# Optimization experiments

Measured on AMD Instinct MI355X. Metric: run time of the kernel, lower is better.

Reference implementation:

```python
import jax, jax.numpy as jnp
import numpy as np

TQ, TK, H, HEADS = 2048, 2048, 1024, 16

def setup_inputs() -> dict:
    key = jax.random.key(0)
    ks = jax.random.split(key, 11)
    s = 1.0 / np.sqrt(H).astype(np.float32)
    return {
        "Q": jax.random.normal(ks[0], (TQ, H), jnp.float32),
        "K": jax.random.normal(ks[1], (TK, H), jnp.float32),
        "V": jax.random.normal(ks[2], (TK, H), jnp.float32),
        "Wq": jax.random.normal(ks[3], (H, H), jnp.float32) * s,
        "bq": jax.random.normal(ks[4], (H,), jnp.float32) * s,
        "Wk": jax.random.normal(ks[5], (H, H), jnp.float32) * s,
        "bk": jax.random.normal(ks[6], (H,), jnp.float32) * s,
        "Wv": jax.random.normal(ks[7], (H, H), jnp.float32) * s,
        "bv": jax.random.normal(ks[8], (H,), jnp.float32) * s,
        # linear_out: nn.Linear(num_heads, 1) -> weight [num_heads], bias scalar
        "Wo": jax.random.normal(ks[9], (HEADS,), jnp.float32) / np.sqrt(HEADS).astype(np.float32),
        "bo": jax.random.normal(ks[10], (), jnp.float32) / np.sqrt(HEADS).astype(np.float32),
    }

def reference(Q, K, V, Wq, bq, Wk, bk, Wv, bv, Wo, bo):
    heads = Wo.shape[0]
    # relu(linear) projections
    Q_l = jax.nn.relu(Q @ Wq.T + bq)            # [Tq, H]
    K_l = jax.nn.relu(K @ Wk.T + bk)            # [Tk, H]
    V_l = jax.nn.relu(V @ Wv.T + bv)            # [Tk, H]
    Tq, Hd = Q_l.shape
    Tk = K_l.shape[0]
    d = Hd // heads                              # head dim
    Qh = Q_l.reshape(Tq, heads, d)               # split heads (torch split+cat over dim0)
    Kh = K_l.reshape(Tk, heads, d)
    # per-head scaled scores: [Tq, Tk, heads]
    scale = np.float32(1.0 / np.sqrt(d))
    scores = jnp.einsum('qhd,khd->qkh', Qh, Kh) * scale
    # learned linear combine over heads -> [Tq, Tk]
    logits = scores @ Wo + bo
    attn = jax.nn.softmax(logits, axis=1)        # softmax over Tk
    out = attn @ V_l                             # [Tq, H]
    return out, attn.T                           # attention.transpose(1,0) -> [Tk, Tq]
```

## Files before the change

kernel.cpp:

```cpp
#include <hip/hip_runtime.h>
#include <stdint.h>


#define TQ 2048
#define TK 2048
#define HD 1024

#define DEVI __device__ __forceinline__

typedef __attribute__((ext_vector_type(8))) short bf16x8;
typedef __attribute__((ext_vector_type(4))) float f32x4;
typedef __attribute__((ext_vector_type(4))) unsigned short u16x4;

DEVI unsigned short f2bf(float f) {
  uint32_t u = __builtin_bit_cast(uint32_t, f);
  u += 0x7FFFu + ((u >> 16) & 1u);
  return (unsigned short)(u >> 16);
}
DEVI float bf2f(unsigned short h) {
  uint32_t u = ((uint32_t)h) << 16;
  return __builtin_bit_cast(float, u);
}
DEVI void gload_lds16(const void* g, void* l) {
  __builtin_amdgcn_global_load_lds((const __attribute__((address_space(1))) void*)g,
                                   (__attribute__((address_space(3))) void*)l,
                                   16, 0, 0);
}
template<int N> DEVI void wait_vm() { asm volatile("s_waitcnt vmcnt(%0)" :: "n"(N) : "memory"); }
DEVI void wait_lgkm0() { asm volatile("s_waitcnt lgkmcnt(0)" ::: "memory"); }
#define SBAR() __builtin_amdgcn_s_barrier()

DEVI void stageT(const unsigned short* __restrict__ A, const unsigned short* __restrict__ B,
                 int lda, int ldb, int k0, unsigned short* buf, int tid) {
#pragma unroll
  for (int i = 0; i < 2; i++) {
    int c = i * 512 + tid;
    int r = c >> 3;
    int cs = (c & 7) ^ (r & 7);
    gload_lds16(A + (size_t)r * lda + k0 + cs * 8, buf + c * 8);
  }
#pragma unroll
  for (int i = 0; i < 2; i++) {
    int c = i * 512 + tid;
    int r = c >> 3;
    int cs = (c & 7) ^ (r & 7);
    gload_lds16(B + (size_t)r * ldb + k0 + cs * 8, buf + 8192 + c * 8);
  }
}

DEVI void computeT(const unsigned short* lA, const unsigned short* lB, f32x4 (*acc)[2],
                   int wr, int wc, int l15, int hi) {
#pragma unroll
  for (int kk = 0; kk < 2; kk++) {
    bf16x8 af[4], bfr[2];
#pragma unroll
    for (int f = 0; f < 4; f++) {
      int ra = wr * 64 + f * 16 + l15;
      int ca = (kk * 4 + hi) ^ (ra & 7);
      af[f] = *(const bf16x8*)(lA + ra * 64 + ca * 8);
    }
#pragma unroll
    for (int f = 0; f < 2; f++) {
      int rb = wc * 32 + f * 16 + l15;
      int cb = (kk * 4 + hi) ^ (rb & 7);
      bfr[f] = *(const bf16x8*)(lB + rb * 64 + cb * 8);
    }
#pragma unroll
    for (int fm = 0; fm < 4; fm++)
#pragma unroll
      for (int fn = 0; fn < 2; fn++)
        acc[fm][fn] = __builtin_amdgcn_mfma_f32_16x16x32_bf16(af[fm], bfr[fn], acc[fm][fn], 0, 0, 0);
  }
}

template<int NKT>
DEVI void mfma_pipeline(const unsigned short* __restrict__ A, const unsigned short* __restrict__ B,
                        int lda, int ldb, unsigned short* lds, f32x4 (*acc)[2]) {
  const int tid = threadIdx.x;
  const int lane = tid & 63, wave = tid >> 6;
  const int l15 = lane & 15, hi = lane >> 4;
  const int wr = wave >> 2, wc = wave & 3;

#pragma unroll
  for (int i = 0; i < 4; i++)
#pragma unroll
    for (int j = 0; j < 2; j++) acc[i][j] = (f32x4)(0.0f);

  stageT(A, B, lda, ldb, 0, lds, tid);
  stageT(A, B, lda, ldb, 64, lds + 16384, tid);

#pragma unroll 1
  for (int t = 0; t < NKT; ++t) {
    if (t < NKT - 1) wait_vm<4>();
    else wait_vm<0>();
    SBAR();
    unsigned short* buf = lds + (t & 1) * 16384;
    __builtin_amdgcn_s_setprio(1);
    computeT(buf, buf + 8192, acc, wr, wc, l15, hi);
    __builtin_amdgcn_s_setprio(0);
    wait_lgkm0();
    SBAR();
    if (t + 2 < NKT) stageT(A, B, lda, ldb, (t + 2) * 64, buf, tid);
  }
}

__global__ __launch_bounds__(512, 4)
void gemm_proj(const unsigned short* __restrict__ Qb, const unsigned short* __restrict__ Kb,
               const unsigned short* __restrict__ Vb,
               const unsigned short* __restrict__ Wqb, const unsigned short* __restrict__ Wkb,
               const unsigned short* __restrict__ Wvb,
               const float* __restrict__ bq, const float* __restrict__ bk,
               const float* __restrict__ bv, const float* __restrict__ Wo,
               unsigned short* __restrict__ Ql, unsigned short* __restrict__ Ks,
               unsigned short* __restrict__ VT) {
  __shared__ __align__(16) unsigned short lds[2 * 16384];
  const int bid = blockIdx.x;
  const int x = bid & 7, j = bid >> 3;
  const int bmz = x * 6 + (j >> 3);
  const int bn = j & 7;
  const int z = bmz >> 4;
  const int bm = bmz & 15;

  const unsigned short* A = (z == 0) ? Qb : (z == 1) ? Kb : Vb;
  const unsigned short* B = (z == 0) ? Wqb : (z == 1) ? Wkb : Wvb;
  const float* bias = (z == 0) ? bq : (z == 1) ? bk : bv;

  f32x4 acc[4][2];
  mfma_pipeline<16>(A + (size_t)bm * 128 * HD, B + (size_t)bn * 128 * HD, HD, HD, lds, acc);

  const int tid = threadIdx.x;
  const int lane = tid & 63, wave = tid >> 6;
  const int wr = wave >> 2, wc = wave & 3;
  const int l15 = lane & 15, hi = lane >> 4;
  const int row0 = bm * 128 + wr * 64;
  const int col0 = bn * 128 + wc * 32;

  if (z == 2) {
    unsigned short (*T)[132] = reinterpret_cast<unsigned short (*)[132]>(lds);
#pragma unroll
    for (int fm = 0; fm < 4; fm++)
#pragma unroll
      for (int fn = 0; fn < 2; fn++) {
        int cl = wc * 32 + fn * 16 + l15;
        float b = bias[bn * 128 + cl];
#pragma unroll
        for (int i = 0; i < 4; i++)
          T[cl][wr * 64 + fm * 16 + hi * 4 + i] = f2bf(fmaxf(acc[fm][fn][i] + b, 0.0f));
      }
    __syncthreads();
#pragma unroll
    for (int i = 0; i < 8; i++) {
      int h = i * 512 + tid;
      int c = h >> 5;
      int rq = h & 31;
      u16x4 v = *(const u16x4*)(&T[c][rq * 4]);
      *(u16x4*)(VT + (size_t)(bn * 128 + c) * TK + bm * 128 + rq * 4) = v;
    }
  } else {
#pragma unroll
    for (int fm = 0; fm < 4; fm++)
#pragma unroll
      for (int fn = 0; fn < 2; fn++) {
        int cg = col0 + fn * 16 + l15;
        int rg = row0 + fm * 16 + hi * 4;
        float b = bias[cg];
        if (z == 1) {
          float s = 0.125f * Wo[cg >> 6];
#pragma unroll
          for (int i = 0; i < 4; i++)
            Ks[(size_t)(rg + i) * HD + cg] = f2bf(fmaxf(acc[fm][fn][i] + b, 0.0f) * s);
        } else {
#pragma unroll
          for (int i = 0; i < 4; i++)
            Ql[(size_t)(rg + i) * HD + cg] = f2bf(fmaxf(acc[fm][fn][i] + b, 0.0f));
        }
      }
  }
}

__global__ __launch_bounds__(512, 4)
void gemm_logits(const unsigned short* __restrict__ Ql, const unsigned short* __restrict__ Ks,
                 float* __restrict__ C) {
  __shared__ __align__(16) unsigned short lds[2 * 16384];
  const int bid = blockIdx.x;
  const int x = bid & 7, j = bid >> 3;
  const int bm = (x & 3) * 4 + (j >> 3);
  const int bn = (x >> 2) * 8 + (j & 7);

  f32x4 acc[4][2];
  mfma_pipeline<16>(Ql + (size_t)bm * 128 * HD, Ks + (size_t)bn * 128 * HD, HD, HD, lds, acc);

  const int tid = threadIdx.x;
  const int lane = tid & 63, wave = tid >> 6;
  const int wr = wave >> 2, wc = wave & 3;
  const int l15 = lane & 15, hi = lane >> 4;
  const int row0 = bm * 128 + wr * 64;
  const int col0 = bn * 128 + wc * 32;
#pragma unroll
  for (int fm = 0; fm < 4; fm++)
#pragma unroll
    for (int fn = 0; fn < 2; fn++) {
      int cg = col0 + fn * 16 + l15;
      int rg = row0 + fm * 16 + hi * 4;
#pragma unroll
      for (int i = 0; i < 4; i++)
        C[(size_t)(rg + i) * TK + cg] = acc[fm][fn][i];
    }
}

__global__ __launch_bounds__(512, 4)
void pv_and_transpose(const unsigned short* __restrict__ attnb, const unsigned short* __restrict__ VT,
                      float* __restrict__ outp, float* __restrict__ attnT) {
  __shared__ __align__(16) unsigned short lds[2 * 16384];
  const int bid = blockIdx.x;
  const int tid = threadIdx.x;
  if (bid < 128) {
    const int x = bid & 7, j = bid >> 3;
    const int bm = (x & 3) * 4 + (j >> 2);
    const int bn = (x >> 2) * 4 + (j & 3);
    f32x4 acc[4][2];
    mfma_pipeline<32>(attnb + (size_t)bm * 128 * TK, VT + (size_t)bn * 128 * TK,
                      TK, TK, lds, acc);
    const int lane = tid & 63, wave = tid >> 6;
    const int wr = wave >> 2, wc = wave & 3;
    const int l15 = lane & 15, hi = lane >> 4;
    const int row0 = bm * 128 + wr * 64;
    const int col0 = bn * 128 + wc * 32;
#pragma unroll
    for (int fm = 0; fm < 4; fm++)
#pragma unroll
      for (int fn = 0; fn < 2; fn++) {
        int cg = col0 + fn * 16 + l15;
        int rg = row0 + fm * 16 + hi * 4;
#pragma unroll
        for (int i = 0; i < 4; i++)
          outp[(size_t)(rg + i) * HD + cg] = acc[fm][fn][i];
      }
  } else {
    unsigned short (*tile)[68] = reinterpret_cast<unsigned short (*)[68]>(lds);
    const int q0 = bid - 128;
    const int tr = (q0 >> 5) * 64;
    const int tc = (q0 & 31) * 64;
#pragma unroll
    for (int i = 0; i < 2; i++) {
      int q = i * 512 + tid;
      int r = q >> 4;
      int c4 = (q & 15) * 4;
      u16x4 v = *(const u16x4*)(attnb + (size_t)(tr + r) * TK + tc + c4);
      *(u16x4*)(&tile[r][c4]) = v;
    }
    __syncthreads();
#pragma unroll
    for (int i = 0; i < 2; i++) {
      int q = i * 512 + tid;
      int c = q >> 4;
      int r4 = (q & 15) * 4;
      f32x4 o;
#pragma unroll
      for (int jx = 0; jx < 4; jx++) o[jx] = bf2f(tile[r4 + jx][c]);
      *(f32x4*)(attnT + (size_t)(tc + c) * TQ + tr + r4) = o;
    }
  }
}

__global__ __launch_bounds__(256)
void softmax_k(const float* __restrict__ logits, unsigned short* __restrict__ attnb) {
  const int row = blockIdx.x;
  const int tid = threadIdx.x;
  const int lane = tid & 63;
  const int wave = tid >> 6;
  const float* lr = logits + (size_t)row * TK;

  f32x4 v0 = *(const f32x4*)(lr + tid * 8);
  f32x4 v1 = *(const f32x4*)(lr + tid * 8 + 4);
  float x[8];
#pragma unroll
  for (int j = 0; j < 4; j++) { x[j] = v0[j]; x[4 + j] = v1[j]; }

  float m = x[0];
#pragma unroll
  for (int j = 1; j < 8; j++) m = fmaxf(m, x[j]);
  for (int o = 32; o > 0; o >>= 1) m = fmaxf(m, __shfl_xor(m, o));
  __shared__ float redm[4], reds[4];
  if (lane == 0) redm[wave] = m;
  __syncthreads();
  m = fmaxf(fmaxf(redm[0], redm[1]), fmaxf(redm[2], redm[3]));

  const float L2E = 1.44269504088896341f;
  float e[8];
  float s = 0.0f;
#pragma unroll
  for (int j = 0; j < 8; j++) { e[j] = exp2f((x[j] - m) * L2E); s += e[j]; }
  for (int o = 32; o > 0; o >>= 1) s += __shfl_xor(s, o);
  if (lane == 0) reds[wave] = s;
  __syncthreads();
  s = reds[0] + reds[1] + reds[2] + reds[3];
  float inv = 1.0f / s;

  unsigned short* ar = attnb + (size_t)row * TK;
  u16x4 o0, o1;
#pragma unroll
  for (int j = 0; j < 4; j++) { o0[j] = f2bf(e[j] * inv); o1[j] = f2bf(e[4 + j] * inv); }
  *(u16x4*)(ar + tid * 8) = o0;
  *(u16x4*)(ar + tid * 8 + 4) = o1;
}

__global__ __launch_bounds__(256)
void cvt6x(const float* __restrict__ Q, const float* __restrict__ K, const float* __restrict__ V,
           const float* __restrict__ Wq, const float* __restrict__ Wk, const float* __restrict__ Wv,
           unsigned short* __restrict__ Qb, unsigned short* __restrict__ Kb,
           unsigned short* __restrict__ Vb, unsigned short* __restrict__ Wqb,
           unsigned short* __restrict__ Wkb, unsigned short* __restrict__ Wvb) {
  const int bid = blockIdx.x;
  const int tid = threadIdx.x;
  if (bid < 6144) {
    const int x = bid & 7, k = bid >> 3;
    const int rb = x * 6 + (k % 6);
    const int s = k / 6;
    const int m = rb >> 4;
    const int r0 = (rb & 15) * 128;
    const float* src = (m == 0) ? Q : (m == 1) ? K : V;
    unsigned short* dst = (m == 0) ? Qb : (m == 1) ? Kb : Vb;
    const int idx4 = r0 * 256 + s * 256 + tid;
    f32x4 v = *(const f32x4*)(src + idx4 * 4);
    u16x4 o;
#pragma unroll
    for (int jj = 0; jj < 4; jj++) o[jj] = f2bf(v[jj]);
    *(u16x4*)(dst + idx4 * 4) = o;
  } else {
    const int w = bid - 6144;
    const int m = w >> 8;
    const int b = w & 255;
    const float* src = (m == 0) ? Wq : (m == 1) ? Wk : Wv;
    unsigned short* dst = (m == 0) ? Wqb : (m == 1) ? Wkb : Wvb;
#pragma unroll
    for (int u = 0; u < 4; u++) {
      const int idx4 = b * 1024 + u * 256 + tid;
      f32x4 v = *(const f32x4*)(src + idx4 * 4);
      u16x4 o;
#pragma unroll
      for (int jj = 0; jj < 4; jj++) o[jj] = f2bf(v[jj]);
      *(u16x4*)(dst + idx4 * 4) = o;
    }
  }
}

extern "C" void kernel_launch(void* const* d_in, const int* in_sizes, int n_in,
                              void* d_out, int out_size, void* d_ws, size_t ws_size,
                              hipStream_t stream) {
  const float* Q  = (const float*)d_in[0];
  const float* K  = (const float*)d_in[1];
  const float* V  = (const float*)d_in[2];
  const float* Wq = (const float*)d_in[3];
  const float* bq = (const float*)d_in[4];
  const float* Wk = (const float*)d_in[5];
  const float* bk = (const float*)d_in[6];
  const float* Wv = (const float*)d_in[7];
  const float* bv = (const float*)d_in[8];
  const float* Wo = (const float*)d_in[9];

  uint8_t* w = (uint8_t*)d_ws;
  unsigned short* Qb  = (unsigned short*)(w + 0);
  unsigned short* Kb  = (unsigned short*)(w + 4194304);
  unsigned short* Vb  = (unsigned short*)(w + 8388608);
  unsigned short* Wqb = (unsigned short*)(w + 12582912);
  unsigned short* Wkb = (unsigned short*)(w + 14680064);
  unsigned short* Wvb = (unsigned short*)(w + 16777216);
  unsigned short* Ql  = (unsigned short*)(w + 18874368);
  unsigned short* Ks  = (unsigned short*)(w + 23068672);
  unsigned short* VT  = (unsigned short*)(w + 27262976);
  float*          logits = (float*)(w + 31457280);
  unsigned short* attnb  = (unsigned short*)(w + 48234496);

  float* outp  = (float*)d_out;
  float* attnT = outp + (size_t)TQ * HD;

  cvt6x<<<dim3(6912), dim3(256), 0, stream>>>(Q, K, V, Wq, Wk, Wv,
                                              Qb, Kb, Vb, Wqb, Wkb, Wvb);

  gemm_proj<<<dim3(384), dim3(512), 0, stream>>>(Qb, Kb, Vb, Wqb, Wkb, Wvb,
                                                 bq, bk, bv, Wo, Ql, Ks, VT);

  gemm_logits<<<dim3(256), dim3(512), 0, stream>>>(Ql, Ks, logits);

  softmax_k<<<dim3(TQ), dim3(256), 0, stream>>>(logits, attnb);

  pv_and_transpose<<<dim3(1152), dim3(512), 0, stream>>>(attnb, VT, outp, attnT);
}
```

Before: 73.92 us.

## Split-K the PV GEMM into two partials and reduce alongside transpose

The attention-times-V GEMM previously ran on only 128 blocks over the full K=2048. It now splits K into two halves across 256 blocks, each writing an fp32 partial into scratch that reuses the Qb/Kb/Vb area. A separate kernel then does the bf16 attention transpose and sums the two partials into the output. This raises GPU occupancy for the GEMM at the cost of an extra kernel launch and roughly 24 MB of additional partial-sum traffic.

```diff
diff --git a/kernel.cpp b/kernel.cpp
--- a/kernel.cpp
+++ b/kernel.cpp
@@ -209,38 +209,49 @@
 }
 
 __global__ __launch_bounds__(512, 4)
-void pv_and_transpose(const unsigned short* __restrict__ attnb, const unsigned short* __restrict__ VT,
-                      float* __restrict__ outp, float* __restrict__ attnT) {
+void gemm_pv(const unsigned short* __restrict__ attnb, const unsigned short* __restrict__ VT,
+             float* __restrict__ part) {
   __shared__ __align__(16) unsigned short lds[2 * 16384];
   const int bid = blockIdx.x;
-  const int tid = threadIdx.x;
-  if (bid < 128) {
-    const int x = bid & 7, j = bid >> 3;
-    const int bm = (x & 3) * 4 + (j >> 2);
-    const int bn = (x >> 2) * 4 + (j & 3);
-    f32x4 acc[4][2];
-    mfma_pipeline<32>(attnb + (size_t)bm * 128 * TK, VT + (size_t)bn * 128 * TK,
-                      TK, TK, lds, acc);
-    const int lane = tid & 63, wave = tid >> 6;
-    const int wr = wave >> 2, wc = wave & 3;
-    const int l15 = lane & 15, hi = lane >> 4;
-    const int row0 = bm * 128 + wr * 64;
-    const int col0 = bn * 128 + wc * 32;
-#pragma unroll
-    for (int fm = 0; fm < 4; fm++)
-#pragma unroll
-      for (int fn = 0; fn < 2; fn++) {
-        int cg = col0 + fn * 16 + l15;
-        int rg = row0 + fm * 16 + hi * 4;
-#pragma unroll
-        for (int i = 0; i < 4; i++)
-          outp[(size_t)(rg + i) * HD + cg] = acc[fm][fn][i];
-      }
-  } else {
-    unsigned short (*tile)[68] = reinterpret_cast<unsigned short (*)[68]>(lds);
-    const int q0 = bid - 128;
-    const int tr = (q0 >> 5) * 64;
-    const int tc = (q0 & 31) * 64;
+  const int ks = bid >> 7;
+  const int inner = bid & 127;
+  const int x = inner & 7, j = inner >> 3;
+  const int bm = (x & 3) * 4 + (j >> 2);
+  const int bn = (x >> 2) * 4 + (j & 3);
+
+  f32x4 acc[4][2];
+  mfma_pipeline<16>(attnb + (size_t)bm * 128 * TK + ks * 1024,
+                    VT + (size_t)bn * 128 * TK + ks * 1024, TK, TK, lds, acc);
+
+  float* Cp = part + (size_t)ks * TQ * HD;
+  const int tid = threadIdx.x;
+  const int lane = tid & 63, wave = tid >> 6;
+  const int wr = wave >> 2, wc = wave & 3;
+  const int l15 = lane & 15, hi = lane >> 4;
+  const int row0 = bm * 128 + wr * 64;
+  const int col0 = bn * 128 + wc * 32;
+#pragma unroll
+  for (int fm = 0; fm < 4; fm++)
+#pragma unroll
+    for (int fn = 0; fn < 2; fn++) {
+      int cg = col0 + fn * 16 + l15;
+      int rg = row0 + fm * 16 + hi * 4;
+#pragma unroll
+      for (int i = 0; i < 4; i++)
+        Cp[(size_t)(rg + i) * HD + cg] = acc[fm][fn][i];
+    }
+}
+
+__global__ __launch_bounds__(512)
+void trans_reduce(const unsigned short* __restrict__ attnb, float* __restrict__ attnT,
+                  const float* __restrict__ p0, const float* __restrict__ p1,
+                  float* __restrict__ outp) {
+  __shared__ unsigned short tile[64][68];
+  const int bid = blockIdx.x;
+  const int tid = threadIdx.x;
+  if (bid < 1024) {
+    const int tr = (bid >> 5) * 64;
+    const int tc = (bid & 31) * 64;
 #pragma unroll
     for (int i = 0; i < 2; i++) {
       int q = i * 512 + tid;
@@ -259,6 +270,18 @@
 #pragma unroll
       for (int jx = 0; jx < 4; jx++) o[jx] = bf2f(tile[r4 + jx][c]);
       *(f32x4*)(attnT + (size_t)(tc + c) * TQ + tr + r4) = o;
+    }
+  } else {
+    const int b = bid - 1024;
+#pragma unroll
+    for (int u = 0; u < 2; u++) {
+      int i = (b * 1024 + u * 512 + tid);
+      f32x4 a = *(const f32x4*)(p0 + (size_t)i * 4);
+      f32x4 c = *(const f32x4*)(p1 + (size_t)i * 4);
+      f32x4 o;
+#pragma unroll
+      for (int jx = 0; jx < 4; jx++) o[jx] = a[jx] + c[jx];
+      *(f32x4*)(outp + (size_t)i * 4) = o;
     }
   }
 }
@@ -371,6 +394,8 @@
   unsigned short* VT  = (unsigned short*)(w + 27262976);
   float*          logits = (float*)(w + 31457280);
   unsigned short* attnb  = (unsigned short*)(w + 48234496);
+  float* p0 = (float*)(w + 0);
+  float* p1 = (float*)(w + 8388608);
 
   float* outp  = (float*)d_out;
   float* attnT = outp + (size_t)TQ * HD;
@@ -385,5 +410,7 @@
 
   softmax_k<<<dim3(TQ), dim3(256), 0, stream>>>(logits, attnb);
 
-  pv_and_transpose<<<dim3(1152), dim3(512), 0, stream>>>(attnb, VT, outp, attnT);
-}
+  gemm_pv<<<dim3(256), dim3(512), 0, stream>>>(attnb, VT, p0);
+
+  trans_reduce<<<dim3(1536), dim3(512), 0, stream>>>(attnb, attnT, p0, p1, outp);
+}
```

After: 76.04 us. 2.9% more time.
